# Performance work log

Measured on AMD Instinct MI355X. Metric: run time of the kernel, lower is better.

Reference implementation:

```python
import jax, jax.numpy as jnp
import numpy as np

B, L, H, W = 4, 5000, 256, 256
C_IN, DIM_LOI, N_PTS0, N_PTS1, DIM_FC, N_OUT_LINE = 256, 128, 32, 8, 1024, 2500
SCALE = N_PTS0 // N_PTS1  # MaxPool1d kernel/stride


def setup_inputs() -> dict:
    key = jax.random.key(0)
    ks = jax.random.split(key, 8)
    feature = jax.random.normal(ks[0], (B, C_IN, H, W), jnp.float32)
    # line endpoints in pixel coords of the 256x256 feature map
    lines = jax.random.uniform(ks[1], (B, L, 2, 2), jnp.float32) * (H - 1)
    s = lambda fan: 1.0 / np.sqrt(fan)
    fc1_w = (jax.random.normal(ks[2], (DIM_LOI, C_IN), jnp.float32) * s(C_IN))
    fc1_b = jnp.zeros((DIM_LOI,), jnp.float32)
    w1 = jax.random.normal(ks[3], (DIM_LOI * N_PTS1, DIM_FC), jnp.float32) * s(DIM_LOI * N_PTS1)
    b1 = jnp.zeros((DIM_FC,), jnp.float32)
    w2 = jax.random.normal(ks[4], (DIM_FC, DIM_FC), jnp.float32) * s(DIM_FC)
    b2 = jnp.zeros((DIM_FC,), jnp.float32)
    w3 = jax.random.normal(ks[5], (DIM_FC, 4), jnp.float32) * s(DIM_FC)
    b3 = jnp.zeros((4,), jnp.float32)
    return dict(feature=feature, lines=lines, fc1_w=fc1_w, fc1_b=fc1_b,
                w1=w1, b1=b1, w2=w2, b2=b2, w3=w3, b3=b3)


def reference(feature, lines, fc1_w, fc1_b, w1, b1, w2, b2, w3, b3):
    # fc1: 1x1 conv  [B,C_IN,H,W] -> [B,DIM_LOI,H,W]
    x = jnp.einsum('bchw,oc->bohw', feature, fc1_w) + fc1_b[None, :, None, None]

    # sample N_PTS0 points along each line (lerp between endpoints), minus 0.5
    lam = jnp.linspace(0.0, 1.0, N_PTS0, dtype=feature.dtype)[None, None, :, None]
    p = lines[:, :, 0:1, :] * lam + lines[:, :, 1:2, :] * (1.0 - lam) - 0.5  # [B,L,P,2]
    px, py = p[..., 0], p[..., 1]  # px indexes H (rows), py indexes W (cols)
    px0 = jnp.clip(jnp.floor(px), 0.0, H - 1.0)
    py0 = jnp.clip(jnp.floor(py), 0.0, W - 1.0)
    px1 = jnp.clip(px0 + 1.0, 0.0, H - 1.0)
    py1 = jnp.clip(py0 + 1.0, 0.0, W - 1.0)
    ix0, iy0 = px0.astype(jnp.int32), py0.astype(jnp.int32)
    ix1, iy1 = px1.astype(jnp.int32), py1.astype(jnp.int32)
    idx00 = ix0 * W + iy0
    idx10 = ix1 * W + iy0
    idx01 = ix0 * W + iy1
    idx11 = ix1 * W + iy1
    w00 = (px1 - px) * (py1 - py)
    w10 = (px - px0) * (py1 - py)
    w01 = (px1 - px) * (py - py0)
    w11 = (px - px0) * (py - py0)

    def gather_one(fmap, i00, i10, i01, i11, g00, g10, g01, g11):
        f = fmap.reshape(DIM_LOI, H * W)
        g = lambda idx: f[:, idx.reshape(-1)].reshape(DIM_LOI, L, N_PTS0)
        return g(i00) * g00 + g(i10) * g10 + g(i01) * g01 + g(i11) * g11

    xp = jax.vmap(gather_one)(x, idx00, idx10, idx01, idx11, w00, w10, w01, w11)
    # xp: [B, DIM_LOI, L, N_PTS0] -> maxpool along points -> [B, DIM_LOI, L, N_PTS1]
    xp = xp.reshape(B, DIM_LOI, L, N_PTS1, SCALE).max(-1)
    # reshape like torch: [N, DIM_LOI, N_PTS1] -> [N, DIM_LOI*N_PTS1] (channel-major)
    feat = xp.transpose(0, 2, 1, 3).reshape(B, L, DIM_LOI * N_PTS1)

    # fc2 MLP -> 4 logits
    h = jax.nn.relu(feat @ w1 + b1)
    h = jax.nn.relu(h @ w2 + b2)
    logits = h @ w3 + b3  # [B, L, 4]
    s = jax.nn.softmax(logits, axis=-1)

    # threshold conditions
    keep = ((s[..., 1] > 0.25) | (s[..., 2] > 0.25) | (s[..., 3] > 0.25)) & (s[..., 0] < 0.25)

    def select(p0, s0, m):
        cnt = m.sum()
        key = jnp.where(m, jnp.argmax(s0, -1), -1)  # masked-out get -1 -> sorted last
        order = jnp.argsort(-key)  # stable desc sort of argmax class
        idx = order[jnp.arange(N_OUT_LINE) % jnp.maximum(cnt, 1)]
        lo = jnp.where(cnt > 0, p0[idx], 0.0)
        so = jnp.where(cnt > 0, s0[idx], 0.0)
        return lo, so

    lines_out, score_out = jax.vmap(select)(lines, s, keep)
    return lines_out, score_out, s
```

## Files before the change

kernel.cpp:

```cpp
#include <hip/hip_runtime.h>
#include <cstdint>
#include <cstddef>

#define B_     4
#define L_     5000
#define H_     256
#define W_     256
#define HW_    65536
#define CIN_   256
#define DLOI_  128
#define NPTS0_ 32
#define NPTS1_ 8
#define DFC_   1024
#define NOUT_  2500
#define M_     (B_*L_)
#define MPAD_  20096
#define NBAND_ 157

typedef _Float16 f16;
typedef _Float16 f16x4 __attribute__((ext_vector_type(4)));
typedef _Float16 f16x8 __attribute__((ext_vector_type(8)));
typedef float    f32x4 __attribute__((ext_vector_type(4)));

__device__ __forceinline__ void gload16(const void* g, void* l) {
  __builtin_amdgcn_global_load_lds(
      (const __attribute__((address_space(1))) void*)g,
      (__attribute__((address_space(3))) void*)l, 16, 0, 0);
}

__global__ __launch_bounds__(256) void k_wsplit(const float* __restrict__ src,
                                                f16* __restrict__ h,
                                                f16* __restrict__ l) {
  int i = (blockIdx.x * 256 + threadIdx.x) * 4;
  float4 v = *(const float4*)(src + i);
  f16 h0 = (f16)v.x, h1 = (f16)v.y, h2 = (f16)v.z, h3 = (f16)v.w;
  *(f16x4*)(h + i) = (f16x4){h0, h1, h2, h3};
  *(f16x4*)(l + i) = (f16x4){(f16)(v.x - (float)h0), (f16)(v.y - (float)h1),
                             (f16)(v.z - (float)h2), (f16)(v.w - (float)h3)};
}

__global__ __launch_bounds__(256) void k_conv_mfma(const float* __restrict__ fin,
                                                   const f16* __restrict__ wh,
                                                   const f16* __restrict__ wl,
                                                   const float* __restrict__ bias,
                                                   float* __restrict__ xout) {
  __shared__ f16 lds[16384];
  const int t = threadIdx.x;
  const int P0 = blockIdx.x * 128;
  const int b  = P0 >> 16;
  const int ph0 = P0 & 65535;
  const int lane = t & 63, wave = t >> 6;
  const int quad = lane >> 4, lo = lane & 15;
  const int wm = wave >> 1, wn = wave & 1;

  const int c_base = (t & 7) * 4;
  const int p = (t >> 3) * 4;
  const size_t fbase = (size_t)b * CIN_ * HW_ + (size_t)ph0 + p;

  const int srow = t >> 2;
  const int skb  = (t & 3) * 16;
  const char* gBh = (const char*)wh + (size_t)srow * 512 + skb;
  const char* gBl = (const char*)wl + (size_t)srow * 512 + skb;
  char* ldsB = (char*)lds + t * 16;

  f32x4 acc[4][4];
  #pragma unroll
  for (int mt = 0; mt < 4; mt++)
    #pragma unroll
    for (int nt = 0; nt < 4; nt++) acc[mt][nt] = (f32x4){0.f, 0.f, 0.f, 0.f};

  float4 av[4], nv[4];
  #pragma unroll
  for (int j = 0; j < 4; j++)
    av[j] = *(const float4*)(fin + fbase + (size_t)(c_base + j) * HW_);

  for (int kc = 0; kc < 8; kc++) {
    const size_t bko = (size_t)kc * 64;
    gload16(gBh + bko,         ldsB + 16384);
    gload16(gBh + 32768 + bko, ldsB + 16384 + 4096);
    gload16(gBl + bko,         ldsB + 24576);
    gload16(gBl + 32768 + bko, ldsB + 24576 + 4096);

    #pragma unroll
    for (int i = 0; i < 4; i++) {
      f16 hh[4], ll[4];
      #pragma unroll
      for (int j = 0; j < 4; j++) {
        float v = ((const float*)&av[j])[i];
        hh[j] = (f16)v;
        ll[j] = (f16)(v - (float)hh[j]);
      }
      *(f16x4*)(&lds[(p + i) * 32 + c_base])        = (f16x4){hh[0], hh[1], hh[2], hh[3]};
      *(f16x4*)(&lds[4096 + (p + i) * 32 + c_base]) = (f16x4){ll[0], ll[1], ll[2], ll[3]};
    }
    __syncthreads();

    if (kc < 7) {
      #pragma unroll
      for (int j = 0; j < 4; j++)
        nv[j] = *(const float4*)(fin + fbase + (size_t)((kc + 1) * 32 + c_base + j) * HW_);
    }

    f16x8 ah[4], al[4], bh4[4], bl4[4];
    #pragma unroll
    for (int mt = 0; mt < 4; mt++) {
      int row = wm * 64 + mt * 16 + lo;
      ah[mt] = *(const f16x8*)(&lds[row * 32 + quad * 8]);
      al[mt] = *(const f16x8*)(&lds[4096 + row * 32 + quad * 8]);
    }
    #pragma unroll
    for (int nt = 0; nt < 4; nt++) {
      int row = wn * 64 + nt * 16 + lo;
      bh4[nt] = *(const f16x8*)(&lds[8192 + row * 32 + quad * 8]);
      bl4[nt] = *(const f16x8*)(&lds[12288 + row * 32 + quad * 8]);
    }
    #pragma unroll
    for (int mt = 0; mt < 4; mt++)
      #pragma unroll
      for (int nt = 0; nt < 4; nt++) {
        acc[mt][nt] = __builtin_amdgcn_mfma_f32_16x16x32_f16(ah[mt], bh4[nt], acc[mt][nt], 0, 0, 0);
        acc[mt][nt] = __builtin_amdgcn_mfma_f32_16x16x32_f16(ah[mt], bl4[nt], acc[mt][nt], 0, 0, 0);
        acc[mt][nt] = __builtin_amdgcn_mfma_f32_16x16x32_f16(al[mt], bh4[nt], acc[mt][nt], 0, 0, 0);
      }
    __syncthreads();
    #pragma unroll
    for (int j = 0; j < 4; j++) av[j] = nv[j];
  }

  #pragma unroll
  for (int nt = 0; nt < 4; nt++) {
    int col = wn * 64 + nt * 16 + lo;
    float bv = bias[col];
    #pragma unroll
    for (int mt = 0; mt < 4; mt++) {
      int rowb = P0 + wm * 64 + mt * 16 + quad * 4;
      #pragma unroll
      for (int r = 0; r < 4; r++)
        xout[(size_t)(rowb + r) * DLOI_ + col] = acc[mt][nt][r] + bv;
    }
  }
}

__global__ __launch_bounds__(128) void k_sample(const float* __restrict__ x,
                                                const float* __restrict__ lines,
                                                f16* __restrict__ fh,
                                                f16* __restrict__ fl) {
  __shared__ int4   s_off[NPTS0_];
  __shared__ float4 s_wt [NPTS0_];
  const int blk = blockIdx.x;
  const int b = blk / L_;
  const int c = threadIdx.x;
  const float* ln = lines + (size_t)blk * 4;

  if (c < NPTS0_) {
    const float e0x = ln[0], e0y = ln[1], e1x = ln[2], e1y = ln[3];
    const int i = c;
    float lam = (float)i * (1.0f / 31.0f);
    float px = e0x * lam + e1x * (1.f - lam) - 0.5f;
    float py = e0y * lam + e1y * (1.f - lam) - 0.5f;
    float px0 = fminf(fmaxf(floorf(px), 0.f), 255.f);
    float py0 = fminf(fmaxf(floorf(py), 0.f), 255.f);
    float px1 = fminf(px0 + 1.f, 255.f);
    float py1 = fminf(py0 + 1.f, 255.f);
    int ix0 = (int)px0, iy0 = (int)py0, ix1 = (int)px1, iy1 = (int)py1;
    s_wt[i]  = make_float4((px1 - px) * (py1 - py),
                           (px - px0) * (py1 - py),
                           (px1 - px) * (py - py0),
                           (px - px0) * (py - py0));
    s_off[i] = make_int4((ix0 * W_ + iy0) * (DLOI_ * 4),
                         (ix1 * W_ + iy0) * (DLOI_ * 4),
                         (ix0 * W_ + iy1) * (DLOI_ * 4),
                         (ix1 * W_ + iy1) * (DLOI_ * 4));
  }
  __syncthreads();

  const char* xbc = (const char*)(x + (size_t)b * HW_ * DLOI_) + c * 4;
  f16x8 vh, vl;
  for (int q = 0; q < NPTS1_; q++) {
    float m = -1e30f;
    #pragma unroll
    for (int r = 0; r < 4; r++) {
      const int i = q * 4 + r;
      const int4   o = s_off[i];
      const float4 w = s_wt[i];
      float v = w.x * *(const float*)(xbc + o.x)
              + w.y * *(const float*)(xbc + o.y)
              + w.z * *(const float*)(xbc + o.z)
              + w.w * *(const float*)(xbc + o.w);
      m = fmaxf(m, v);
    }
    f16 h = (f16)m;
    vh[q] = h;
    vl[q] = (f16)(m - (float)h);
  }
  *(f16x8*)(fh + (size_t)blk * DFC_ + c * 8) = vh;
  *(f16x8*)(fl + (size_t)blk * DFC_ + c * 8) = vl;
}

__global__ __launch_bounds__(256) void k_tsplit(const float* __restrict__ Wsrc,
                                                f16* __restrict__ Th,
                                                f16* __restrict__ Tl) {
  __shared__ float tile[32][33];
  const int bj = blockIdx.x, bi = blockIdx.y;
  const int tx = threadIdx.x & 31, ty = threadIdx.x >> 5;
  #pragma unroll
  for (int r = ty; r < 32; r += 8)
    tile[r][tx] = Wsrc[(size_t)(bi * 32 + r) * 1024 + bj * 32 + tx];
  __syncthreads();
  #pragma unroll
  for (int r = ty; r < 32; r += 8) {
    float v = tile[tx][r];
    f16 h = (f16)v;
    size_t o = (size_t)(bj * 32 + r) * 1024 + bi * 32 + tx;
    Th[o] = h;
    Tl[o] = (f16)(v - (float)h);
  }
}

#define BKT_    32
#define NTT_    (DFC_/BKT_)
#define SLOT_B_ 49152
#define AH_O_   0
#define AL_O_   8192
#define BH_O_   16384
#define BL_O_   32768

template <bool SPLIT_OUT>
__global__ __launch_bounds__(512, 2) void k_gemm_f16x3(
    const f16* __restrict__ Ah, const f16* __restrict__ Al,
    const f16* __restrict__ Bh, const f16* __restrict__ Bl,
    const float* __restrict__ bias,
    f16* __restrict__ Oh, f16* __restrict__ Ol,
    const float* __restrict__ w3, float* __restrict__ part) {
  __shared__ f16 lds[3 * SLOT_B_ / 2];
  char* ldsc = (char*)lds;

  const int orig = blockIdx.x;
  const int xcd = orig & 7, bidx = orig >> 3;
  const int qq = 628 >> 3, rr = 628 & 7;
  const int wg = (xcd < rr ? xcd * (qq + 1) : rr * (qq + 1) + (xcd - rr) * qq) + bidx;
  const int band = wg >> 2;
  const int nb   = wg & 3;
  const int r0 = band * 128;
  const int n0 = nb * 256;

  const int t = threadIdx.x;
  const int lane = t & 63, wave = t >> 6;
  const int quad = lane >> 4, lo = lane & 15;
  const int wm = wave >> 2, wn = wave & 3;

  const uint32_t usA  = (uint32_t)t ^ (((uint32_t)t >> 3) & 7);
  const uint32_t uB1  = (uint32_t)t + 512u;
  const uint32_t usB1 = uB1 ^ ((uB1 >> 3) & 7);
  const size_t sA  = (size_t)(usA  >> 2) * 2048 + (size_t)(usA  & 3) * 16;
  const size_t sB1 = (size_t)(usB1 >> 2) * 2048 + (size_t)(usB1 & 3) * 16;

  const char* gAh  = (const char*)Ah + (size_t)r0 * 2048 + sA;
  const char* gAl  = (const char*)Al + (size_t)r0 * 2048 + sA;
  const char* gBh0 = (const char*)Bh + (size_t)n0 * 2048 + sA;
  const char* gBh1 = (const char*)Bh + (size_t)n0 * 2048 + sB1;
  const char* gBl0 = (const char*)Bl + (size_t)n0 * 2048 + sA;
  const char* gBl1 = (const char*)Bl + (size_t)n0 * 2048 + sB1;

  const int dAh  = AH_O_ + t * 16;
  const int dAl  = AL_O_ + t * 16;
  const int dBh0 = BH_O_ + t * 16;
  const int dBh1 = BH_O_ + 8192 + t * 16;
  const int dBl0 = BL_O_ + t * 16;
  const int dBl1 = BL_O_ + 8192 + t * 16;

  int roffA[4], roffB[4];
  #pragma unroll
  for (int mt = 0; mt < 4; mt++) {
    int r = wm * 64 + mt * 16 + lo;
    roffA[mt] = (((r * 4 + quad) ^ ((r >> 1) & 7)) << 4);
  }
  #pragma unroll
  for (int nt = 0; nt < 4; nt++) {
    int r = wn * 64 + nt * 16 + lo;
    roffB[nt] = (((r * 4 + quad) ^ ((r >> 1) & 7)) << 4);
  }

  f32x4 acc[4][4];
  #pragma unroll
  for (int mt = 0; mt < 4; mt++)
    #pragma unroll
    for (int nt = 0; nt < 4; nt++) acc[mt][nt] = (f32x4){0.f, 0.f, 0.f, 0.f};

  gload16(gAh,        ldsc + dAh);
  gload16(gAl,        ldsc + dAl);
  gload16(gBh0,       ldsc + dBh0);
  gload16(gBh1,       ldsc + dBh1);
  gload16(gBl0,       ldsc + dBl0);
  gload16(gBl1,       ldsc + dBl1);
  gload16(gAh  + 64,  ldsc + SLOT_B_ + dAh);
  gload16(gAl  + 64,  ldsc + SLOT_B_ + dAl);
  gload16(gBh0 + 64,  ldsc + SLOT_B_ + dBh0);
  gload16(gBh1 + 64,  ldsc + SLOT_B_ + dBh1);
  gload16(gBl0 + 64,  ldsc + SLOT_B_ + dBl0);
  gload16(gBl1 + 64,  ldsc + SLOT_B_ + dBl1);
  asm volatile("s_waitcnt vmcnt(6)" ::: "memory");
  __builtin_amdgcn_s_barrier();

  int cur = 0, stg = 2;
  for (int tt = 0; tt < NTT_; ++tt) {
    const char* sc = ldsc + cur * SLOT_B_;
    char* sw = ldsc + stg * SLOT_B_;
    const size_t go = (size_t)tt * 64 + 128;
    const bool pf = (tt + 2 < NTT_);

    if (pf) {
      gload16(gAh  + go, sw + dAh);
      gload16(gAl  + go, sw + dAl);
      gload16(gBh0 + go, sw + dBh0);
      gload16(gBh1 + go, sw + dBh1);
      gload16(gBl0 + go, sw + dBl0);
      gload16(gBl1 + go, sw + dBl1);
    }

    f16x8 ah[4], bh[4], al[4], bl[4];
    #pragma unroll
    for (int mt = 0; mt < 4; mt++)
      ah[mt] = *(const f16x8*)(sc + AH_O_ + roffA[mt]);
    #pragma unroll
    for (int nt = 0; nt < 4; nt++)
      bh[nt] = *(const f16x8*)(sc + BH_O_ + roffB[nt]);
    #pragma unroll
    for (int mt = 0; mt < 4; mt++)
      al[mt] = *(const f16x8*)(sc + AL_O_ + roffA[mt]);
    #pragma unroll
    for (int nt = 0; nt < 4; nt++)
      bl[nt] = *(const f16x8*)(sc + BL_O_ + roffB[nt]);

    __builtin_amdgcn_s_setprio(1);
    #pragma unroll
    for (int mt = 0; mt < 4; mt++)
      #pragma unroll
      for (int nt = 0; nt < 4; nt++)
        acc[mt][nt] = __builtin_amdgcn_mfma_f32_16x16x32_f16(ah[mt], bh[nt], acc[mt][nt], 0, 0, 0);
    #pragma unroll
    for (int mt = 0; mt < 4; mt++)
      #pragma unroll
      for (int nt = 0; nt < 4; nt++)
        acc[mt][nt] = __builtin_amdgcn_mfma_f32_16x16x32_f16(al[mt], bh[nt], acc[mt][nt], 0, 0, 0);
    #pragma unroll
    for (int mt = 0; mt < 4; mt++)
      #pragma unroll
      for (int nt = 0; nt < 4; nt++)
        acc[mt][nt] = __builtin_amdgcn_mfma_f32_16x16x32_f16(ah[mt], bl[nt], acc[mt][nt], 0, 0, 0);
    __builtin_amdgcn_s_setprio(0);

    if (tt < NTT_ - 2)       asm volatile("s_waitcnt vmcnt(6)" ::: "memory");
    else if (tt == NTT_ - 2) asm volatile("s_waitcnt vmcnt(0)" ::: "memory");
    __builtin_amdgcn_s_barrier();

    cur = (cur == 2) ? 0 : cur + 1;
    stg = (stg == 2) ? 0 : stg + 1;
  }

  if (SPLIT_OUT) {
    char* ep = ldsc + wave * 16384;
    #pragma unroll
    for (int mt = 0; mt < 4; mt++)
      #pragma unroll
      for (int nt = 0; nt < 4; nt++) {
        const int col = n0 + wn * 64 + nt * 16 + lo;
        const float bv = bias[col];
        const int col_l = nt * 16 + lo;
        #pragma unroll
        for (int r = 0; r < 4; r++) {
          const int rl = mt * 16 + quad * 4 + r;
          float v = fmaxf(acc[mt][nt][r] + bv, 0.f);
          f16 h = (f16)v;
          f16 lw = (f16)(v - (float)h);
          const int byte = rl * 128 + ((((col_l >> 3) ^ (rl & 7)) << 4)) + (col_l & 7) * 2;
          *(f16*)(ep + byte) = h;
          *(f16*)(ep + 8192 + byte) = lw;
        }
      }
    asm volatile("s_waitcnt lgkmcnt(0)" ::: "memory");
    __builtin_amdgcn_sched_barrier(0);
    const int r8 = lane >> 3;
    const int ck = lane & 7;
    #pragma unroll
    for (int g = 0; g < 8; g++) {
      const int rl = g * 8 + r8;
      const int grow = r0 + wm * 64 + rl;
      const int swz = ((ck ^ (rl & 7)) << 4);
      f16x8 vh = *(const f16x8*)(ep + rl * 128 + swz);
      f16x8 vl = *(const f16x8*)(ep + 8192 + rl * 128 + swz);
      if (grow < M_) {
        const size_t gb = (size_t)grow * 2048 + (size_t)(n0 + wn * 64) * 2 + ck * 16;
        *(f16x8*)((char*)Oh + gb) = vh;
        *(f16x8*)((char*)Ol + gb) = vl;
      }
    }
  } else {
    const int slot = nb * 4 + wn;
    #pragma unroll
    for (int mt = 0; mt < 4; mt++) {
      float p[4][4];
      #pragma unroll
      for (int r = 0; r < 4; r++)
        #pragma unroll
        for (int j = 0; j < 4; j++) p[r][j] = 0.f;
      #pragma unroll
      for (int nt = 0; nt < 4; nt++) {
        const int col = n0 + wn * 64 + nt * 16 + lo;
        const float bv = bias[col];
        float4 wv = *(const float4*)(w3 + col * 4);
        #pragma unroll
        for (int r = 0; r < 4; r++) {
          float v = fmaxf(acc[mt][nt][r] + bv, 0.f);
          p[r][0] = fmaf(v, wv.x, p[r][0]);
          p[r][1] = fmaf(v, wv.y, p[r][1]);
          p[r][2] = fmaf(v, wv.z, p[r][2]);
          p[r][3] = fmaf(v, wv.w, p[r][3]);
        }
      }
      #pragma unroll
      for (int r = 0; r < 4; r++)
        #pragma unroll
        for (int j = 0; j < 4; j++) {
          p[r][j] += __shfl_xor(p[r][j], 1);
          p[r][j] += __shfl_xor(p[r][j], 2);
          p[r][j] += __shfl_xor(p[r][j], 4);
          p[r][j] += __shfl_xor(p[r][j], 8);
        }
      if (lo == 0) {
        const int rowb = r0 + wm * 64 + mt * 16 + quad * 4;
        #pragma unroll
        for (int r = 0; r < 4; r++)
          *(float4*)(part + ((size_t)slot * MPAD_ + rowb + r) * 4) =
              make_float4(p[r][0], p[r][1], p[r][2], p[r][3]);
      }
    }
  }
}

__global__ __launch_bounds__(256) void k_head2(const float* __restrict__ part,
                                               const float* __restrict__ b3,
                                               float* __restrict__ s_out,
                                               int* __restrict__ key_out) {
  const int row = blockIdx.x * 256 + threadIdx.x;
  if (row >= M_) return;
  float l0 = b3[0], l1 = b3[1], l2 = b3[2], l3 = b3[3];
  #pragma unroll
  for (int sl = 0; sl < 16; sl++) {
    float4 p = *(const float4*)(part + ((size_t)sl * MPAD_ + row) * 4);
    l0 += p.x; l1 += p.y; l2 += p.z; l3 += p.w;
  }
  float mx = fmaxf(fmaxf(l0, l1), fmaxf(l2, l3));
  float e0 = expf(l0 - mx), e1 = expf(l1 - mx), e2 = expf(l2 - mx), e3 = expf(l3 - mx);
  float inv = 1.f / (e0 + e1 + e2 + e3);
  float s0 = e0 * inv, s1 = e1 * inv, s2 = e2 * inv, s3 = e3 * inv;
  *(float4*)(s_out + (size_t)row * 4) = make_float4(s0, s1, s2, s3);
  bool keep = ((s1 > 0.25f) || (s2 > 0.25f) || (s3 > 0.25f)) && (s0 < 0.25f);
  int am = 0; float best = s0;
  if (s1 > best) { best = s1; am = 1; }
  if (s2 > best) { best = s2; am = 2; }
  if (s3 > best) { best = s3; am = 3; }
  key_out[row] = keep ? am : -1;
}

__global__ __launch_bounds__(1024) void k_select(const int* __restrict__ key,
                                                 const float* __restrict__ lines,
                                                 const float* __restrict__ s,
                                                 float* __restrict__ out_lines,
                                                 float* __restrict__ out_score) {
  __shared__ int s_ord[L_];
  __shared__ int s_scan[1024];
  __shared__ int s_tot[5];
  const int b = blockIdx.x;
  const int t = threadIdx.x;
  const int base_l = t * 5;
  int cls[5];
  int c[5] = {0, 0, 0, 0, 0};
  #pragma unroll
  for (int i = 0; i < 5; i++) {
    int l = base_l + i;
    int cl = -1;
    if (l < L_) {
      int k = key[b * L_ + l];
      cl = (k < 0) ? 4 : (3 - k);
      c[cl]++;
    }
    cls[i] = cl;
  }
  int pf[5];
  for (int cc = 0; cc < 5; cc++) {
    s_scan[t] = c[cc];
    __syncthreads();
    for (int off = 1; off < 1024; off <<= 1) {
      int add = (t >= off) ? s_scan[t - off] : 0;
      __syncthreads();
      s_scan[t] += add;
      __syncthreads();
    }
    pf[cc] = s_scan[t] - c[cc];
    if (t == 1023) s_tot[cc] = s_scan[1023];
    __syncthreads();
  }
  int basec[5];
  basec[0] = 0;
  #pragma unroll
  for (int cc = 1; cc < 5; cc++) basec[cc] = basec[cc - 1] + s_tot[cc - 1];
  int run[5] = {0, 0, 0, 0, 0};
  #pragma unroll
  for (int i = 0; i < 5; i++) {
    if (cls[i] >= 0) {
      int cl = cls[i];
      int pos = basec[cl] + pf[cl] + run[cl];
      run[cl]++;
      s_ord[pos] = base_l + i;
    }
  }
  const int cnt = L_ - s_tot[4];
  __syncthreads();
  for (int j = t; j < NOUT_; j += 1024) {
    float4 lv = make_float4(0.f, 0.f, 0.f, 0.f);
    float4 sv = make_float4(0.f, 0.f, 0.f, 0.f);
    if (cnt > 0) {
      int idx = s_ord[j % cnt];
      lv = *(const float4*)(lines + (size_t)(b * L_ + idx) * 4);
      sv = *(const float4*)(s + (size_t)(b * L_ + idx) * 4);
    }
    *(float4*)(out_lines + (size_t)(b * NOUT_ + j) * 4) = lv;
    *(float4*)(out_score + (size_t)(b * NOUT_ + j) * 4) = sv;
  }
}

extern "C" void kernel_launch(void* const* d_in, const int* in_sizes, int n_in,
                              void* d_out, int out_size, void* d_ws, size_t ws_size,
                              hipStream_t stream) {
  const float* feature = (const float*)d_in[0];
  const float* lines   = (const float*)d_in[1];
  const float* fc1_w   = (const float*)d_in[2];
  const float* fc1_b   = (const float*)d_in[3];
  const float* w1      = (const float*)d_in[4];
  const float* b1      = (const float*)d_in[5];
  const float* w2      = (const float*)d_in[6];
  const float* b2      = (const float*)d_in[7];
  const float* w3      = (const float*)d_in[8];
  const float* b3      = (const float*)d_in[9];

  float* out_lines = (float*)d_out;
  float* out_score = out_lines + B_ * NOUT_ * 4;
  float* s_out     = out_score + B_ * NOUT_ * 4;

  char* ws = (char*)d_ws;
  float* x    = (float*)(ws);
  f16*   h1h  = (f16*)(ws);
  f16*   h1l  = (f16*)(ws + 41156608ull);
  float* part = (float*)(ws + 82313216ull);
  f16*   fh   = (f16*)(ws + 134217728ull);
  f16*   fl   = (f16*)(ws + 134217728ull + 41156608ull);
  f16*   wt1h = (f16*)(ws + 216530944ull);
  f16*   wt1l = (f16*)(ws + 216530944ull + 2097152ull);
  f16*   wt2h = (f16*)(ws + 216530944ull + 2ull * 2097152ull);
  f16*   wt2l = (f16*)(ws + 216530944ull + 3ull * 2097152ull);
  int*   keys = (int*)(ws + 224919552ull);
  f16*   wc_h = (f16*)(ws + 224999552ull);
  f16*   wc_l = (f16*)(ws + 224999552ull + 65536ull);

  k_wsplit<<<dim3(32), 256, 0, stream>>>(fc1_w, wc_h, wc_l);
  k_tsplit<<<dim3(32, 32), 256, 0, stream>>>(w1, wt1h, wt1l);
  k_tsplit<<<dim3(32, 32), 256, 0, stream>>>(w2, wt2h, wt2l);
  k_conv_mfma<<<dim3((B_ * HW_) / 128), 256, 0, stream>>>(feature, wc_h, wc_l, fc1_b, x);
  k_sample<<<dim3(M_), 128, 0, stream>>>(x, lines, fh, fl);
  k_gemm_f16x3<true><<<dim3(628), 512, 0, stream>>>(
      fh, fl, wt1h, wt1l, b1, h1h, h1l, nullptr, nullptr);
  k_gemm_f16x3<false><<<dim3(628), 512, 0, stream>>>(
      h1h, h1l, wt2h, wt2l, b2, nullptr, nullptr, w3, part);
  k_head2<<<dim3((M_ + 255) / 256), 256, 0, stream>>>(part, b3, s_out, keys);
  k_select<<<dim3(B_), 1024, 0, stream>>>(keys, lines, s_out, out_lines, out_score);
}
```

Baseline: 876.0 us.

## Sort lines spatially by Morton cell and map sample blocks per XCD

Adds a kernel that buckets each batch's lines by the Morton-ordered 32x32 cell of their midpoint, producing a permutation. The sampling kernel remaps block indices so each XCD processes a contiguous run of spatially sorted lines and writes results back to the original row. This aims to improve L2/cache hit rates for the bilinear gathers from the large conv output. It adds a small extra kernel launch and reuses the keys buffer for the permutation.

```diff
diff --git a/kernel.cpp b/kernel.cpp
--- a/kernel.cpp
+++ b/kernel.cpp
@@ -39,6 +39,46 @@
                              (f16)(v.z - (float)h2), (f16)(v.w - (float)h3)};
 }
 
+__global__ __launch_bounds__(1024) void k_order(const float* __restrict__ lines,
+                                                int* __restrict__ perm) {
+  __shared__ int hist[64];
+  __shared__ int off[64];
+  const int b = blockIdx.x;
+  const int t = threadIdx.x;
+  if (t < 64) hist[t] = 0;
+  __syncthreads();
+  int mycell[5];
+  #pragma unroll
+  for (int i = 0; i < 5; i++) {
+    const int l = t * 5 + i;
+    int cell = -1;
+    if (l < L_) {
+      const float* ln = lines + (size_t)(b * L_ + l) * 4;
+      float mx = 0.5f * (ln[0] + ln[2]);
+      float my = 0.5f * (ln[1] + ln[3]);
+      int cx = min(max((int)mx, 0), 255) >> 5;
+      int cy = min(max((int)my, 0), 255) >> 5;
+      cell = (cx & 1) | ((cy & 1) << 1) | ((cx & 2) << 1) | ((cy & 2) << 2)
+           | ((cx & 4) << 2) | ((cy & 4) << 3);
+      atomicAdd(&hist[cell], 1);
+    }
+    mycell[i] = cell;
+  }
+  __syncthreads();
+  if (t == 0) {
+    int s = 0;
+    for (int c = 0; c < 64; c++) { off[c] = s; s += hist[c]; }
+  }
+  __syncthreads();
+  #pragma unroll
+  for (int i = 0; i < 5; i++) {
+    if (mycell[i] >= 0) {
+      int slot = atomicAdd(&off[mycell[i]], 1);
+      perm[b * L_ + slot] = t * 5 + i;
+    }
+  }
+}
+
 __global__ __launch_bounds__(256) void k_conv_mfma(const float* __restrict__ fin,
                                                    const f16* __restrict__ wh,
                                                    const f16* __restrict__ wl,
@@ -143,14 +183,17 @@
 
 __global__ __launch_bounds__(128) void k_sample(const float* __restrict__ x,
                                                 const float* __restrict__ lines,
+                                                const int* __restrict__ perm,
                                                 f16* __restrict__ fh,
                                                 f16* __restrict__ fl) {
   __shared__ int4   s_off[NPTS0_];
   __shared__ float4 s_wt [NPTS0_];
-  const int blk = blockIdx.x;
-  const int b = blk / L_;
+  const int blk0 = blockIdx.x;
+  const int s = (blk0 & 7) * (M_ / 8) + (blk0 >> 3);
+  const int b = s / L_;
+  const int row = b * L_ + perm[s];
   const int c = threadIdx.x;
-  const float* ln = lines + (size_t)blk * 4;
+  const float* ln = lines + (size_t)row * 4;
 
   if (c < NPTS0_) {
     const float e0x = ln[0], e0y = ln[1], e1x = ln[2], e1y = ln[3];
@@ -193,8 +236,8 @@
     vh[q] = h;
     vl[q] = (f16)(m - (float)h);
   }
-  *(f16x8*)(fh + (size_t)blk * DFC_ + c * 8) = vh;
-  *(f16x8*)(fl + (size_t)blk * DFC_ + c * 8) = vl;
+  *(f16x8*)(fh + (size_t)row * DFC_ + c * 8) = vh;
+  *(f16x8*)(fl + (size_t)row * DFC_ + c * 8) = vl;
 }
 
 __global__ __launch_bounds__(256) void k_tsplit(const float* __restrict__ Wsrc,
@@ -563,11 +606,12 @@
   f16*   wc_h = (f16*)(ws + 224999552ull);
   f16*   wc_l = (f16*)(ws + 224999552ull + 65536ull);
 
+  k_order<<<dim3(B_), 1024, 0, stream>>>(lines, keys);
   k_wsplit<<<dim3(32), 256, 0, stream>>>(fc1_w, wc_h, wc_l);
   k_tsplit<<<dim3(32, 32), 256, 0, stream>>>(w1, wt1h, wt1l);
   k_tsplit<<<dim3(32, 32), 256, 0, stream>>>(w2, wt2h, wt2l);
   k_conv_mfma<<<dim3((B_ * HW_) / 128), 256, 0, stream>>>(feature, wc_h, wc_l, fc1_b, x);
-  k_sample<<<dim3(M_), 128, 0, stream>>>(x, lines, fh, fl);
+  k_sample<<<dim3(M_), 128, 0, stream>>>(x, lines, keys, fh, fl);
   k_gemm_f16x3<true><<<dim3(628), 512, 0, stream>>>(
       fh, fl, wt1h, wt1l, b1, h1h, h1l, nullptr, nullptr);
   k_gemm_f16x3<false><<<dim3(628), 512, 0, stream>>>(
```

Measured after the change: 870.5 us. No clear change (-0.6%).
